# Kernel tuning notes

Measured on AMD Instinct MI355X. Metric: run time of the kernel, lower is better.

## Reference

```python
import jax, jax.numpy as jnp
import numpy as np
import math

B, S, D, H = 4, 2048, 2048, 16
DK = D // H
NEG = -1e9


def _rope_factor(seq_len, d_k, dtype):
    # Faithful to source: apply_rope computes x*cos + x*sin = x*(cos+sin).
    # freqs = exp(arange(0, d_k, 2) * -(ln(10000)/d_k)); each freq is repeated
    # twice along the feature dim so the factor broadcasts over d_k.
    pos = jnp.arange(seq_len, dtype=jnp.float32)
    freqs = jnp.exp(jnp.arange(0, d_k, 2, dtype=jnp.float32) * (-(math.log(10000.0) / d_k)))
    freqs = jnp.repeat(freqs, 2)  # [d_k]
    ang = pos[:, None] * freqs[None, :]  # [S, d_k]
    return (jnp.cos(ang) + jnp.sin(ang)).astype(dtype)


def setup_inputs() -> dict:
    key = jax.random.key(0)
    k1, k2, k3 = jax.random.split(key, 3)
    x = jax.random.normal(k1, (B, S, D), dtype=jnp.float32)
    attention_mask = jnp.ones((B, S), dtype=jnp.float32)
    w_qkv = jax.random.normal(k2, (3 * D, D), dtype=jnp.float32) * 0.02
    w_o = jax.random.normal(k3, (D, D), dtype=jnp.float32) * 0.02
    return {"x": x, "attention_mask": attention_mask, "w_qkv": w_qkv, "w_o": w_o}


def reference(x, attention_mask, w_qkv, w_o):
    b, s, d = x.shape
    h, dk = H, DK
    qkv = x @ w_qkv.T  # [b, s, 3d]
    qkv = qkv.reshape(b, s, 3, h, dk).transpose(2, 0, 3, 1, 4)  # [3, b, h, s, dk]
    q, k, v = qkv[0], qkv[1], qkv[2]
    rf = _rope_factor(s, dk, x.dtype)  # [s, dk]
    q = q * rf[None, None]
    k = k * rf[None, None]
    scores = jnp.einsum('bhqd,bhkd->bhqk', q, k) / math.sqrt(dk)
    causal = jnp.tril(jnp.ones((s, s), dtype=bool))
    scores = jnp.where(causal[None, None], scores, NEG)
    scores = scores + (1.0 - attention_mask)[:, None, None, :] * NEG
    attn = jax.nn.softmax(scores, axis=-1)  # dropout p=0 (eval) -> identity
    out = jnp.einsum('bhqk,bhkd->bhqd', attn, v)
    out = out.transpose(0, 2, 1, 3).reshape(b, s, d)
    output = out @ w_o.T
    return (output, attn)
```

## Files before the change

### kernel.cpp

```cpp
#include <hip/hip_runtime.h>

typedef unsigned short u16;
typedef __bf16 bf16x8 __attribute__((ext_vector_type(8)));
typedef float f32x4 __attribute__((ext_vector_type(4)));

#define DEV __device__ __forceinline__

static constexpr int Bb = 4, Ss = 2048, Dd = 2048, Hh = 16, DK = 128;

DEV u16 f2bf(float f){
  unsigned u = __builtin_bit_cast(unsigned, f);
  return (u16)((u + 0x7fffu + ((u >> 16) & 1u)) >> 16);
}

DEV void async16(const void* g, void* l){
  __builtin_amdgcn_global_load_lds(
      (const __attribute__((address_space(1))) unsigned int*)(unsigned long long)g,
      (__attribute__((address_space(3))) unsigned int*)(unsigned int)(unsigned long long)l,
      16, 0, 0);
}

DEV bf16x8 ldsv(const u16* p){ return *(const bf16x8*)p; }

DEV bf16x8 ldswz(const u16* base, int row, int cb){
  return *(const bf16x8*)((const char*)base + row * 256 + (cb ^ ((row & 7) << 4)));
}

__global__ __launch_bounds__(256) void cvt_kernel(const float* __restrict__ s,
                                                  u16* __restrict__ d, int n4){
  int i = blockIdx.x * 256 + threadIdx.x;
  if (i < n4){
    float4 v = ((const float4*)s)[i];
    ushort4 o;
    o.x = f2bf(v.x); o.y = f2bf(v.y); o.z = f2bf(v.z); o.w = f2bf(v.w);
    ((ushort4*)d)[i] = o;
  }
}

__global__ __launch_bounds__(256) void rope_kernel(float* __restrict__ rf){
  int i = blockIdx.x * 256 + threadIdx.x;
  int s = i >> 7, dk = i & 127;
  float freq = __expf(-(float)(dk & ~1) * 0.0719557841560639344f);
  float a = (float)s * freq;
  rf[i] = cosf(a) + sinf(a);
}

__global__ __launch_bounds__(256) void bias_kernel(const float* __restrict__ mask,
                                                   float* __restrict__ kb, int n){
  int i = blockIdx.x * 256 + threadIdx.x;
  if (i < n) kb[i] = (1.0f - mask[i]) * (-1e9f);
}

DEV void gemm_mainloop(const u16* __restrict__ A, const u16* __restrict__ B,
                       int m0, int n0, int K, u16* As, u16* Bs,
                       int wave, int lane, f32x4 acc[4][4]){
  const int l15 = lane & 15, l4 = lane >> 4;
  const int wm = (wave >> 1) * 64, wn = (wave & 1) * 64;
  for (int k0 = 0; k0 < K; k0 += 32){
    __syncthreads();
#pragma unroll
    for (int i = 0; i < 2; i++){
      const int c = i * 256 + wave * 64 + lane;
      const int r = c >> 2, ci = (c & 3) << 3;
      async16(A + (size_t)(m0 + r) * K + k0 + ci, As + c * 8);
      async16(B + (size_t)(n0 + r) * K + k0 + ci, Bs + c * 8);
    }
    __syncthreads();
    bf16x8 af[4], bv[4];
#pragma unroll
    for (int mi = 0; mi < 4; mi++) af[mi] = ldsv(As + (wm + mi * 16 + l15) * 32 + l4 * 8);
#pragma unroll
    for (int ni = 0; ni < 4; ni++) bv[ni] = ldsv(Bs + (wn + ni * 16 + l15) * 32 + l4 * 8);
#pragma unroll
    for (int mi = 0; mi < 4; mi++)
#pragma unroll
      for (int ni = 0; ni < 4; ni++)
        acc[mi][ni] = __builtin_amdgcn_mfma_f32_16x16x32_bf16(af[mi], bv[ni], acc[mi][ni], 0, 0, 0);
  }
}

__global__ __launch_bounds__(256) void gemm_qkv_kernel(
    const u16* __restrict__ A, const u16* __restrict__ Bw, const float* __restrict__ rf,
    u16* __restrict__ q_out, u16* __restrict__ k_out, u16* __restrict__ vt_out){
  __shared__ u16 As[128 * 32], Bs[128 * 32];
  const int tid = threadIdx.x, wave = tid >> 6, lane = tid & 63;
  const int l15 = lane & 15, l4 = lane >> 4;
  const int m0 = blockIdx.y * 128, n0 = blockIdx.x * 128;
  const int wm = (wave >> 1) * 64, wn = (wave & 1) * 64;
  f32x4 acc[4][4];
  const f32x4 z = {0.f, 0.f, 0.f, 0.f};
#pragma unroll
  for (int mi = 0; mi < 4; mi++)
#pragma unroll
    for (int ni = 0; ni < 4; ni++) acc[mi][ni] = z;

  gemm_mainloop(A, Bw, m0, n0, 2048, As, Bs, wave, lane, acc);

  const int which = n0 >> 11, h = (n0 >> 7) & 15;
  if (which == 2){
#pragma unroll
    for (int mi = 0; mi < 4; mi++){
      int mbase = m0 + wm + mi * 16 + l4 * 4;
      int b = mbase >> 11, s = mbase & 2047;
#pragma unroll
      for (int ni = 0; ni < 4; ni++){
        int dk = wn + ni * 16 + l15;
        ushort4 o;
        o.x = f2bf(acc[mi][ni][0]); o.y = f2bf(acc[mi][ni][1]);
        o.z = f2bf(acc[mi][ni][2]); o.w = f2bf(acc[mi][ni][3]);
        *(ushort4*)(vt_out + ((size_t)(b * Hh + h) * DK + dk) * Ss + s) = o;
      }
    }
  } else {
    u16* dst = which == 0 ? q_out : k_out;
#pragma unroll
    for (int mi = 0; mi < 4; mi++)
#pragma unroll
      for (int r = 0; r < 4; r++){
        int m = m0 + wm + mi * 16 + l4 * 4 + r;
        int b = m >> 11, s = m & 2047;
        size_t rowbase = ((size_t)(b * Hh + h) * Ss + s) * DK;
#pragma unroll
        for (int ni = 0; ni < 4; ni++){
          int dk = wn + ni * 16 + l15;
          float v = acc[mi][ni][r] * rf[s * DK + dk];
          dst[rowbase + dk] = f2bf(v);
        }
      }
  }
}

__global__ __launch_bounds__(256) void gemm_out_kernel(
    const u16* __restrict__ A, const u16* __restrict__ Bw, float* __restrict__ out){
  __shared__ u16 As[128 * 32], Bs[128 * 32];
  const int tid = threadIdx.x, wave = tid >> 6, lane = tid & 63;
  const int l15 = lane & 15, l4 = lane >> 4;
  const int m0 = blockIdx.y * 128, n0 = blockIdx.x * 128;
  const int wm = (wave >> 1) * 64, wn = (wave & 1) * 64;
  f32x4 acc[4][4];
  const f32x4 z = {0.f, 0.f, 0.f, 0.f};
#pragma unroll
  for (int mi = 0; mi < 4; mi++)
#pragma unroll
    for (int ni = 0; ni < 4; ni++) acc[mi][ni] = z;

  gemm_mainloop(A, Bw, m0, n0, 2048, As, Bs, wave, lane, acc);

#pragma unroll
  for (int mi = 0; mi < 4; mi++)
#pragma unroll
    for (int r = 0; r < 4; r++){
      int m = m0 + wm + mi * 16 + l4 * 4 + r;
#pragma unroll
      for (int ni = 0; ni < 4; ni++)
        out[(size_t)m * Dd + n0 + wn + ni * 16 + l15] = acc[mi][ni][r];
    }
}

__global__ __launch_bounds__(256) void attn_kernel(
    const u16* __restrict__ qg, const u16* __restrict__ kg, const u16* __restrict__ vtg,
    const float* __restrict__ kbias, float* __restrict__ attn, u16* __restrict__ obuf){
  __shared__ u16 KV[128 * 128];
  __shared__ u16 Ps[64 * 136];
  __shared__ float m_s[64], l_s[64], a_s[64], red0[64], red1[64];

  const int tid = threadIdx.x, wave = tid >> 6, lane = tid & 63;
  const int l15 = lane & 15, l4 = lane >> 4;
  const int bid = blockIdx.x;
  const int virt = (bid & 7) * 256 + (bid >> 3);
  const int bh = virt >> 5, b = bh >> 4, h = bh & 15;
  const int q0 = (31 - (virt & 31)) << 6;
  const int wq = (wave >> 1) * 32, wk = (wave & 1) * 64;

  const size_t bhoff = (size_t)bh * Ss * DK;
  const u16* qp = qg + bhoff;
  const u16* kp = kg + bhoff;
  const u16* vp = vtg + bhoff;

  bf16x8 qf[2][4];
#pragma unroll
  for (int mi = 0; mi < 2; mi++)
#pragma unroll
    for (int ks = 0; ks < 4; ks++)
      qf[mi][ks] = ldsv(qp + (size_t)(q0 + wq + mi * 16 + l15) * DK + ks * 32 + l4 * 8);

  if (tid < 64){ m_s[tid] = -1e30f; l_s[tid] = 0.f; }

  const int ntiles = (q0 >> 7) + 1;
  const float scale = 0.08838834764831845f;
  const f32x4 z = {0.f, 0.f, 0.f, 0.f};

  for (int t = 0; t < ntiles; t++){
    const int j0 = t << 7;
    __syncthreads();
#pragma unroll
    for (int i = 0; i < 8; i++){
      int c = i * 256 + tid;
      int r = c >> 4, cb = (c & 15) << 4;
      int scb = cb ^ ((r & 7) << 4);
      async16(kp + (size_t)(j0 + r) * DK + (scb >> 1), (char*)KV + (size_t)c * 16);
    }
    __syncthreads();
    f32x4 sacc[2][4];
#pragma unroll
    for (int mi = 0; mi < 2; mi++)
#pragma unroll
      for (int ni = 0; ni < 4; ni++) sacc[mi][ni] = z;
    __builtin_amdgcn_s_setprio(1);
#pragma unroll
    for (int ks = 0; ks < 4; ks++){
      bf16x8 kf[4];
#pragma unroll
      for (int ni = 0; ni < 4; ni++) kf[ni] = ldswz(KV, wk + ni * 16 + l15, ks * 64 + l4 * 16);
#pragma unroll
      for (int mi = 0; mi < 2; mi++)
#pragma unroll
        for (int ni = 0; ni < 4; ni++)
          sacc[mi][ni] = __builtin_amdgcn_mfma_f32_16x16x32_bf16(qf[mi][ks], kf[ni], sacc[mi][ni], 0, 0, 0);
    }
    __builtin_amdgcn_s_setprio(0);
    float kb4[4];
#pragma unroll
    for (int ni = 0; ni < 4; ni++) kb4[ni] = kbias[b * Ss + j0 + wk + ni * 16 + l15];

    float rmx[2][4];
#pragma unroll
    for (int mi = 0; mi < 2; mi++)
#pragma unroll
      for (int r = 0; r < 4; r++) rmx[mi][r] = -3e38f;
#pragma unroll
    for (int mi = 0; mi < 2; mi++)
#pragma unroll
      for (int ni = 0; ni < 4; ni++)
#pragma unroll
        for (int r = 0; r < 4; r++){
          int qi = q0 + wq + mi * 16 + l4 * 4 + r;
          int kj = j0 + wk + ni * 16 + l15;
          float sv = sacc[mi][ni][r] * scale + kb4[ni];
          sv = (kj > qi) ? -1e9f : sv;
          sacc[mi][ni][r] = sv;
          rmx[mi][r] = fmaxf(rmx[mi][r], sv);
        }
#pragma unroll
    for (int d = 1; d < 16; d <<= 1)
#pragma unroll
      for (int mi = 0; mi < 2; mi++)
#pragma unroll
        for (int r = 0; r < 4; r++) rmx[mi][r] = fmaxf(rmx[mi][r], __shfl_xor(rmx[mi][r], d, 64));
    if (l15 == 0){
      float* red = (wave & 1) ? red1 : red0;
#pragma unroll
      for (int mi = 0; mi < 2; mi++)
#pragma unroll
        for (int r = 0; r < 4; r++) red[wq + mi * 16 + l4 * 4 + r] = rmx[mi][r];
    }
    __syncthreads();
    if (tid < 64){
      float mo = m_s[tid];
      float mn = fmaxf(mo, fmaxf(red0[tid], red1[tid]));
      m_s[tid] = mn;
      a_s[tid] = __expf(mo - mn);
    }
    __syncthreads();
    float es[2][4];
#pragma unroll
    for (int mi = 0; mi < 2; mi++)
#pragma unroll
      for (int r = 0; r < 4; r++){
        float mn = m_s[wq + mi * 16 + l4 * 4 + r];
        float e = 0.f;
#pragma unroll
        for (int ni = 0; ni < 4; ni++) e += __expf(sacc[mi][ni][r] - mn);
        es[mi][r] = e;
      }
#pragma unroll
    for (int d = 1; d < 16; d <<= 1)
#pragma unroll
      for (int mi = 0; mi < 2; mi++)
#pragma unroll
        for (int r = 0; r < 4; r++) es[mi][r] += __shfl_xor(es[mi][r], d, 64);
    if (l15 == 0){
      float* red = (wave & 1) ? red1 : red0;
#pragma unroll
      for (int mi = 0; mi < 2; mi++)
#pragma unroll
        for (int r = 0; r < 4; r++) red[wq + mi * 16 + l4 * 4 + r] = es[mi][r];
    }
    __syncthreads();
    if (tid < 64) l_s[tid] = l_s[tid] * a_s[tid] + red0[tid] + red1[tid];
  }
  __syncthreads();
  if (tid < 64) l_s[tid] = 1.0f / l_s[tid];

  f32x4 oacc[2][4];
#pragma unroll
  for (int mi = 0; mi < 2; mi++)
#pragma unroll
    for (int ni = 0; ni < 4; ni++) oacc[mi][ni] = z;

  for (int t = 0; t < ntiles; t++){
    const int j0 = t << 7;
    __syncthreads();
#pragma unroll
    for (int i = 0; i < 8; i++){
      int c = i * 256 + tid;
      int r = c >> 4, cb = (c & 15) << 4;
      int scb = cb ^ ((r & 7) << 4);
      async16(kp + (size_t)(j0 + r) * DK + (scb >> 1), (char*)KV + (size_t)c * 16);
    }
    __syncthreads();
    f32x4 sacc[2][4];
#pragma unroll
    for (int mi = 0; mi < 2; mi++)
#pragma unroll
      for (int ni = 0; ni < 4; ni++) sacc[mi][ni] = z;
    __builtin_amdgcn_s_setprio(1);
#pragma unroll
    for (int ks = 0; ks < 4; ks++){
      bf16x8 kf[4];
#pragma unroll
      for (int ni = 0; ni < 4; ni++) kf[ni] = ldswz(KV, wk + ni * 16 + l15, ks * 64 + l4 * 16);
#pragma unroll
      for (int mi = 0; mi < 2; mi++)
#pragma unroll
        for (int ni = 0; ni < 4; ni++)
          sacc[mi][ni] = __builtin_amdgcn_mfma_f32_16x16x32_bf16(qf[mi][ks], kf[ni], sacc[mi][ni], 0, 0, 0);
    }
    __builtin_amdgcn_s_setprio(0);
    float kb4[4];
#pragma unroll
    for (int ni = 0; ni < 4; ni++) kb4[ni] = kbias[b * Ss + j0 + wk + ni * 16 + l15];
#pragma unroll
    for (int mi = 0; mi < 2; mi++)
#pragma unroll
      for (int r = 0; r < 4; r++){
        int row = wq + mi * 16 + l4 * 4 + r;
        int qi = q0 + row;
        float mn = m_s[row], il = l_s[row];
        size_t abase = ((size_t)bh * Ss + qi) * Ss + j0 + wk;
#pragma unroll
        for (int ni = 0; ni < 4; ni++){
          int kj = j0 + wk + ni * 16 + l15;
          float sv = sacc[mi][ni][r] * scale + kb4[ni];
          sv = (kj > qi) ? -1e9f : sv;
          float p = __expf(sv - mn) * il;
          attn[abase + ni * 16 + l15] = p;
          sacc[mi][ni][r] = p;
        }
      }
    __syncthreads();
#pragma unroll
    for (int i = 0; i < 8; i++){
      int c = i * 256 + tid;
      int r = c >> 4, cb = (c & 15) << 4;
      int scb = cb ^ ((r & 7) << 4);
      async16(vp + (size_t)r * Ss + j0 + (scb >> 1), (char*)KV + (size_t)c * 16);
    }
#pragma unroll
    for (int mi = 0; mi < 2; mi++)
#pragma unroll
      for (int ni = 0; ni < 4; ni++)
#pragma unroll
        for (int r = 0; r < 4; r++){
          int row = wq + mi * 16 + l4 * 4 + r;
          Ps[row * 136 + wk + ni * 16 + l15] = f2bf(sacc[mi][ni][r]);
        }
    __syncthreads();
    __builtin_amdgcn_s_setprio(1);
#pragma unroll
    for (int ks = 0; ks < 4; ks++){
      bf16x8 pf[2], vf[4];
#pragma unroll
      for (int mi = 0; mi < 2; mi++) pf[mi] = ldsv(Ps + (wq + mi * 16 + l15) * 136 + ks * 32 + l4 * 8);
#pragma unroll
      for (int ni = 0; ni < 4; ni++) vf[ni] = ldswz(KV, wk + ni * 16 + l15, ks * 64 + l4 * 16);
#pragma unroll
      for (int mi = 0; mi < 2; mi++)
#pragma unroll
        for (int ni = 0; ni < 4; ni++)
          oacc[mi][ni] = __builtin_amdgcn_mfma_f32_16x16x32_bf16(pf[mi], vf[ni], oacc[mi][ni], 0, 0, 0);
    }
    __builtin_amdgcn_s_setprio(0);
  }

#pragma unroll
  for (int mi = 0; mi < 2; mi++)
#pragma unroll
    for (int r = 0; r < 4; r++){
      int row = wq + mi * 16 + l4 * 4 + r;
      int s = q0 + row;
#pragma unroll
      for (int ni = 0; ni < 4; ni++){
        int dk = wk + ni * 16 + l15;
        obuf[(size_t)(b * Ss + s) * Dd + h * DK + dk] = f2bf(oacc[mi][ni][r]);
      }
    }

  int c0 = ntiles << 7;
  if (c0 < Ss){
    int nf4 = (Ss - c0) >> 2;
    size_t base = ((size_t)bh * Ss + q0) * Ss;
    for (int idx = tid; idx < nf4 * 64; idx += 256){
      int rr = idx / nf4, cc = idx - rr * nf4;
      *(float4*)(attn + base + (size_t)rr * Ss + c0 + cc * 4) = make_float4(0.f, 0.f, 0.f, 0.f);
    }
  }
}

extern "C" void kernel_launch(void* const* d_in, const int* in_sizes, int n_in,
                              void* d_out, int out_size, void* d_ws, size_t ws_size,
                              hipStream_t stream){
  const float* x     = (const float*)d_in[0];
  const float* amask = (const float*)d_in[1];
  const float* wqkv  = (const float*)d_in[2];
  const float* wo    = (const float*)d_in[3];

  float* out  = (float*)d_out;
  float* attn = out + (size_t)Bb * Ss * Dd;

  char* ws = (char*)d_ws;
  u16*  xb    = (u16*)(ws + 0);
  u16*  wqkvb = (u16*)(ws + 33554432ull);
  u16*  wob   = (u16*)(ws + 58720256ull);
  u16*  qb    = (u16*)(ws + 67108864ull);
  u16*  kb    = (u16*)(ws + 100663296ull);
  u16*  vtb   = (u16*)(ws + 134217728ull);
  float* rf   = (float*)(ws + 167772160ull);
  float* kbias= (float*)(ws + 168820736ull);

  cvt_kernel<<<16384, 256, 0, stream>>>(x, xb, 4194304);
  cvt_kernel<<<12288, 256, 0, stream>>>(wqkv, wqkvb, 3145728);
  cvt_kernel<<<4096, 256, 0, stream>>>(wo, wob, 1048576);
  rope_kernel<<<1024, 256, 0, stream>>>(rf);
  bias_kernel<<<32, 256, 0, stream>>>(amask, kbias, Bb * Ss);

  gemm_qkv_kernel<<<dim3(48, 64), 256, 0, stream>>>(xb, wqkvb, rf, qb, kb, vtb);
  attn_kernel<<<dim3(2048), 256, 0, stream>>>(qb, kb, vtb, kbias, attn, xb );
  gemm_out_kernel<<<dim3(16, 64), 256, 0, stream>>>(xb, wob, out);
}
```

Measured before the change: 1.817 ms.

## Prefetch next K/V tile during softmax and merge per-half max/sum reductions

Issues the async load of the next K tile (or the V tile) right after the QK MFMAs, so the global-to-LDS copy overlaps the softmax math instead of sitting behind two barriers. The first pass now computes each half's local max and exp-sum in one step and merges them with rescaling, which removes one barrier and one reduction round per tile. The attention-probability stores are moved after the PV MFMAs so they overlap the next K prefetch. The risks are correctness hazards from reusing the single KV buffer across the new barrier placement, and a small amount of extra exp work in the merge.

New measurement: 1.825 ms. About the same (+0.5%).

```diff
diff --git a/kernel.cpp b/kernel.cpp
--- a/kernel.cpp
+++ b/kernel.cpp
@@ -157,12 +157,33 @@
     }
 }
 
+DEV void stageK(const u16* kp, int j0, u16* KV, int tid){
+#pragma unroll
+  for (int i = 0; i < 8; i++){
+    int c = i * 256 + tid;
+    int r = c >> 4, cb = (c & 15) << 4;
+    int scb = cb ^ ((r & 7) << 4);
+    async16(kp + (size_t)(j0 + r) * DK + (scb >> 1), (char*)KV + (size_t)c * 16);
+  }
+}
+
+DEV void stageV(const u16* vp, int j0, u16* KV, int tid){
+#pragma unroll
+  for (int i = 0; i < 8; i++){
+    int c = i * 256 + tid;
+    int r = c >> 4, cb = (c & 15) << 4;
+    int scb = cb ^ ((r & 7) << 4);
+    async16(vp + (size_t)r * Ss + j0 + (scb >> 1), (char*)KV + (size_t)c * 16);
+  }
+}
+
 __global__ __launch_bounds__(256) void attn_kernel(
     const u16* __restrict__ qg, const u16* __restrict__ kg, const u16* __restrict__ vtg,
     const float* __restrict__ kbias, float* __restrict__ attn, u16* __restrict__ obuf){
   __shared__ u16 KV[128 * 128];
   __shared__ u16 Ps[64 * 136];
-  __shared__ float m_s[64], l_s[64], a_s[64], red0[64], red1[64];
+  __shared__ float m_s[64], l_s[64];
+  __shared__ float redm[2][64], redl[2][64];
 
   const int tid = threadIdx.x, wave = tid >> 6, lane = tid & 63;
   const int l15 = lane & 15, l4 = lane >> 4;
@@ -171,6 +192,7 @@
   const int bh = virt >> 5, b = bh >> 4, h = bh & 15;
   const int q0 = (31 - (virt & 31)) << 6;
   const int wq = (wave >> 1) * 32, wk = (wave & 1) * 64;
+  const int wh = wave & 1;
 
   const size_t bhoff = (size_t)bh * Ss * DK;
   const u16* qp = qg + bhoff;
@@ -190,17 +212,10 @@
   const float scale = 0.08838834764831845f;
   const f32x4 z = {0.f, 0.f, 0.f, 0.f};
 
+  stageK(kp, 0, KV, tid);
   for (int t = 0; t < ntiles; t++){
     const int j0 = t << 7;
     __syncthreads();
-#pragma unroll
-    for (int i = 0; i < 8; i++){
-      int c = i * 256 + tid;
-      int r = c >> 4, cb = (c & 15) << 4;
-      int scb = cb ^ ((r & 7) << 4);
-      async16(kp + (size_t)(j0 + r) * DK + (scb >> 1), (char*)KV + (size_t)c * 16);
-    }
-    __syncthreads();
     f32x4 sacc[2][4];
 #pragma unroll
     for (int mi = 0; mi < 2; mi++)
@@ -219,15 +234,20 @@
           sacc[mi][ni] = __builtin_amdgcn_mfma_f32_16x16x32_bf16(qf[mi][ks], kf[ni], sacc[mi][ni], 0, 0, 0);
     }
     __builtin_amdgcn_s_setprio(0);
+    __syncthreads();
+    {
+      int nxt = (t + 1 < ntiles) ? (j0 + 128) : 0;
+      stageK(kp, nxt, KV, tid);
+    }
     float kb4[4];
 #pragma unroll
     for (int ni = 0; ni < 4; ni++) kb4[ni] = kbias[b * Ss + j0 + wk + ni * 16 + l15];
 
-    float rmx[2][4];
-#pragma unroll
-    for (int mi = 0; mi < 2; mi++)
-#pragma unroll
-      for (int r = 0; r < 4; r++) rmx[mi][r] = -3e38f;
+    float lm[2][4];
+#pragma unroll
+    for (int mi = 0; mi < 2; mi++)
+#pragma unroll
+      for (int r = 0; r < 4; r++) lm[mi][r] = -3e38f;
 #pragma unroll
     for (int mi = 0; mi < 2; mi++)
 #pragma unroll
@@ -239,55 +259,50 @@
           float sv = sacc[mi][ni][r] * scale + kb4[ni];
           sv = (kj > qi) ? -1e9f : sv;
           sacc[mi][ni][r] = sv;
-          rmx[mi][r] = fmaxf(rmx[mi][r], sv);
+          lm[mi][r] = fmaxf(lm[mi][r], sv);
         }
 #pragma unroll
     for (int d = 1; d < 16; d <<= 1)
 #pragma unroll
       for (int mi = 0; mi < 2; mi++)
 #pragma unroll
-        for (int r = 0; r < 4; r++) rmx[mi][r] = fmaxf(rmx[mi][r], __shfl_xor(rmx[mi][r], d, 64));
+        for (int r = 0; r < 4; r++) lm[mi][r] = fmaxf(lm[mi][r], __shfl_xor(lm[mi][r], d, 64));
+    float ls[2][4];
+#pragma unroll
+    for (int mi = 0; mi < 2; mi++)
+#pragma unroll
+      for (int r = 0; r < 4; r++){
+        float e = 0.f;
+#pragma unroll
+        for (int ni = 0; ni < 4; ni++) e += __expf(sacc[mi][ni][r] - lm[mi][r]);
+        ls[mi][r] = e;
+      }
+#pragma unroll
+    for (int d = 1; d < 16; d <<= 1)
+#pragma unroll
+      for (int mi = 0; mi < 2; mi++)
+#pragma unroll
+        for (int r = 0; r < 4; r++) ls[mi][r] += __shfl_xor(ls[mi][r], d, 64);
     if (l15 == 0){
-      float* red = (wave & 1) ? red1 : red0;
-#pragma unroll
-      for (int mi = 0; mi < 2; mi++)
-#pragma unroll
-        for (int r = 0; r < 4; r++) red[wq + mi * 16 + l4 * 4 + r] = rmx[mi][r];
+#pragma unroll
+      for (int mi = 0; mi < 2; mi++)
+#pragma unroll
+        for (int r = 0; r < 4; r++){
+          int row = wq + mi * 16 + l4 * 4 + r;
+          redm[wh][row] = lm[mi][r];
+          redl[wh][row] = ls[mi][r];
+        }
     }
     __syncthreads();
     if (tid < 64){
       float mo = m_s[tid];
-      float mn = fmaxf(mo, fmaxf(red0[tid], red1[tid]));
+      float lm0 = redm[0][tid], lm1 = redm[1][tid];
+      float mn = fmaxf(mo, fmaxf(lm0, lm1));
       m_s[tid] = mn;
-      a_s[tid] = __expf(mo - mn);
-    }
-    __syncthreads();
-    float es[2][4];
-#pragma unroll
-    for (int mi = 0; mi < 2; mi++)
-#pragma unroll
-      for (int r = 0; r < 4; r++){
-        float mn = m_s[wq + mi * 16 + l4 * 4 + r];
-        float e = 0.f;
-#pragma unroll
-        for (int ni = 0; ni < 4; ni++) e += __expf(sacc[mi][ni][r] - mn);
-        es[mi][r] = e;
-      }
-#pragma unroll
-    for (int d = 1; d < 16; d <<= 1)
-#pragma unroll
-      for (int mi = 0; mi < 2; mi++)
-#pragma unroll
-        for (int r = 0; r < 4; r++) es[mi][r] += __shfl_xor(es[mi][r], d, 64);
-    if (l15 == 0){
-      float* red = (wave & 1) ? red1 : red0;
-#pragma unroll
-      for (int mi = 0; mi < 2; mi++)
-#pragma unroll
-        for (int r = 0; r < 4; r++) red[wq + mi * 16 + l4 * 4 + r] = es[mi][r];
-    }
-    __syncthreads();
-    if (tid < 64) l_s[tid] = l_s[tid] * a_s[tid] + red0[tid] + red1[tid];
+      l_s[tid] = l_s[tid] * __expf(mo - mn)
+               + redl[0][tid] * __expf(lm0 - mn)
+               + redl[1][tid] * __expf(lm1 - mn);
+    }
   }
   __syncthreads();
   if (tid < 64) l_s[tid] = 1.0f / l_s[tid];
@@ -301,14 +316,6 @@
   for (int t = 0; t < ntiles; t++){
     const int j0 = t << 7;
     __syncthreads();
-#pragma unroll
-    for (int i = 0; i < 8; i++){
-      int c = i * 256 + tid;
-      int r = c >> 4, cb = (c & 15) << 4;
-      int scb = cb ^ ((r & 7) << 4);
-      async16(kp + (size_t)(j0 + r) * DK + (scb >> 1), (char*)KV + (size_t)c * 16);
-    }
-    __syncthreads();
     f32x4 sacc[2][4];
 #pragma unroll
     for (int mi = 0; mi < 2; mi++)
@@ -327,6 +334,9 @@
           sacc[mi][ni] = __builtin_amdgcn_mfma_f32_16x16x32_bf16(qf[mi][ks], kf[ni], sacc[mi][ni], 0, 0, 0);
     }
     __builtin_amdgcn_s_setprio(0);
+    __syncthreads();
+    stageV(vp, j0, KV, tid);
+
     float kb4[4];
 #pragma unroll
     for (int ni = 0; ni < 4; ni++) kb4[ni] = kbias[b * Ss + j0 + wk + ni * 16 + l15];
@@ -337,34 +347,16 @@
         int row = wq + mi * 16 + l4 * 4 + r;
         int qi = q0 + row;
         float mn = m_s[row], il = l_s[row];
-        size_t abase = ((size_t)bh * Ss + qi) * Ss + j0 + wk;
 #pragma unroll
         for (int ni = 0; ni < 4; ni++){
           int kj = j0 + wk + ni * 16 + l15;
           float sv = sacc[mi][ni][r] * scale + kb4[ni];
           sv = (kj > qi) ? -1e9f : sv;
           float p = __expf(sv - mn) * il;
-          attn[abase + ni * 16 + l15] = p;
           sacc[mi][ni][r] = p;
+          Ps[row * 136 + wk + ni * 16 + l15] = f2bf(p);
         }
       }
-    __syncthreads();
-#pragma unroll
-    for (int i = 0; i < 8; i++){
-      int c = i * 256 + tid;
-      int r = c >> 4, cb = (c & 15) << 4;
-      int scb = cb ^ ((r & 7) << 4);
-      async16(vp + (size_t)r * Ss + j0 + (scb >> 1), (char*)KV + (size_t)c * 16);
-    }
-#pragma unroll
-    for (int mi = 0; mi < 2; mi++)
-#pragma unroll
-      for (int ni = 0; ni < 4; ni++)
-#pragma unroll
-        for (int r = 0; r < 4; r++){
-          int row = wq + mi * 16 + l4 * 4 + r;
-          Ps[row * 136 + wk + ni * 16 + l15] = f2bf(sacc[mi][ni][r]);
-        }
     __syncthreads();
     __builtin_amdgcn_s_setprio(1);
 #pragma unroll
@@ -381,6 +373,19 @@
           oacc[mi][ni] = __builtin_amdgcn_mfma_f32_16x16x32_bf16(pf[mi], vf[ni], oacc[mi][ni], 0, 0, 0);
     }
     __builtin_amdgcn_s_setprio(0);
+    __syncthreads();
+    if (t + 1 < ntiles) stageK(kp, j0 + 128, KV, tid);
+
+#pragma unroll
+    for (int mi = 0; mi < 2; mi++)
+#pragma unroll
+      for (int r = 0; r < 4; r++){
+        int qi = q0 + wq + mi * 16 + l4 * 4 + r;
+        size_t abase = ((size_t)bh * Ss + qi) * Ss + j0 + wk;
+#pragma unroll
+        for (int ni = 0; ni < 4; ni++)
+          attn[abase + ni * 16 + l15] = sacc[mi][ni][r];
+      }
   }
 
 #pragma unroll
```
